# Performance work log

Measured on AMD Instinct MI355X. Metric: run time of the kernel, lower is better.

The kernel has to match this reference:

```python
import jax, jax.numpy as jnp
import numpy as np

N = 20000      # num_nodes / scatter_size
F = 128        # dataset_num_features
H = 8          # heads
HID = 64       # hidden_channels
REP = 512      # represent_features
NCLS = 133     # dataset_num_classes
E = 200000     # num edges (== num synapses)
PTS = 4        # points per synapse
P = E * PTS    # total synapse points

# Eval-mode semantics: dropout = identity; PyG MLP BatchNorm with fresh
# running stats (mean=0, var=1, affine=1/0) = identity. GATConv has no
# edge_dim, so edge_attr does not enter the math (kept as an input for parity).

def _glorot(key, shape):
    fan_in, fan_out = shape[0], shape[-1]
    if len(shape) == 3:  # attention vectors [H, C]: PyG treats as (1, H*C)
        fan_in, fan_out = 1, shape[-2] * shape[-1]
    lim = jnp.sqrt(6.0 / (fan_in + fan_out))
    return jax.random.uniform(key, shape, jnp.float32, -lim, lim)


def setup_inputs() -> dict:
    key = jax.random.key(0)
    ks = jax.random.split(key, 20)
    edge_index = jax.random.randint(ks[0], (2, E), 0, N, dtype=jnp.int32)
    edge_attr = jax.random.normal(ks[1], (E, 1), jnp.float32)
    synapse = jax.random.normal(ks[2], (P, 6), jnp.float32)
    # every synapse (edge) owns PTS points -> no empty segments for max-pool
    synapse_index = (jnp.arange(P, dtype=jnp.int32) // PTS)
    inp = {
        "edge_index": edge_index,
        "edge_attr": edge_attr,
        "synapse": synapse,
        "synapse_index": synapse_index,
        "scatter_size": N,
        # learned node embedding (nn.Parameter, xavier)
        "x_param": _glorot(ks[3], (N, F)),
        # GATConv 1: F -> H*HID
        "W1": _glorot(ks[4], (F, H * HID)),
        "att_src1": _glorot(ks[5], (1, H, HID))[0],
        "att_dst1": _glorot(ks[6], (1, H, HID))[0],
        "b1": jnp.zeros((H * HID,), jnp.float32),
        # GATConv 2: H*HID -> REP, heads=1, concat=False
        "W2": _glorot(ks[7], (H * HID, REP)),
        "att_src2": _glorot(ks[8], (1, 1, REP))[0],
        "att_dst2": _glorot(ks[9], (1, 1, REP))[0],
        "b2": jnp.zeros((REP,), jnp.float32),
        # synapse_encoder MLP([6, 256, 512])
        "We1": _glorot(ks[10], (6, 256)),
        "be1": jnp.zeros((256,), jnp.float32),
        "We2": _glorot(ks[11], (256, 512)),
        "be2": jnp.zeros((512,), jnp.float32),
        # classmodel MLP([1536, 512, 133])
        "Wc1": _glorot(ks[12], (1536, 512)),
        "bc1": jnp.zeros((512,), jnp.float32),
        "Wc2": _glorot(ks[13], (512, NCLS)),
        "bc2": jnp.zeros((NCLS,), jnp.float32),
    }
    return inp


def _gat_conv(x, src, dst, n, W, a_src, a_dst, b, heads, ch, concat):
    # x: [n, Fin]; src/dst already include self-loops (PyG default)
    xl = (x @ W).reshape(n, heads, ch)                 # [n, H, C]
    s = jnp.einsum('nhc,hc->nh', xl, a_src)            # alpha_src
    d = jnp.einsum('nhc,hc->nh', xl, a_dst)            # alpha_dst
    alpha = jax.nn.leaky_relu(s[src] + d[dst], negative_slope=0.2)  # [Ee, H]
    amax = jax.ops.segment_max(alpha, dst, num_segments=n)
    ex = jnp.exp(alpha - amax[dst])
    den = jax.ops.segment_sum(ex, dst, num_segments=n)
    a = ex / (den[dst] + 1e-16)                        # segment softmax
    out = jax.ops.segment_sum(xl[src] * a[:, :, None], dst, num_segments=n)
    out = out.reshape(n, heads * ch) if concat else out.mean(axis=1)
    return out + b


def _scatter_mean(vals, idx, n):
    s = jax.ops.segment_sum(vals, idx, num_segments=n)
    cnt = jax.ops.segment_sum(jnp.ones((vals.shape[0],), vals.dtype), idx, num_segments=n)
    return s / jnp.maximum(cnt, 1.0)[:, None]


def reference(edge_index, edge_attr, synapse, synapse_index, scatter_size,
              x_param, W1, att_src1, att_dst1, b1, W2, att_src2, att_dst2, b2,
              We1, be1, We2, be2, Wc1, bc1, Wc2, bc2):
    n = scatter_size
    loop = jnp.arange(n, dtype=edge_index.dtype)
    src = jnp.concatenate([edge_index[0], loop])   # GATConv adds self-loops
    dst = jnp.concatenate([edge_index[1], loop])

    x = jax.nn.elu(_gat_conv(x_param, src, dst, n, W1, att_src1, att_dst1, b1, H, HID, True))
    x = _gat_conv(x, src, dst, n, W2, att_src2, att_dst2, b2, 1, REP, False)   # [n, REP]

    # global_max_pool over synapse points -> one 6-vec per edge
    x_point = jax.ops.segment_max(synapse, synapse_index, num_segments=E)      # [E, 6]
    x_point = jax.nn.relu(x_point @ We1 + be1) @ We2 + be2                      # [E, 512]

    left = _scatter_mean(x_point, edge_index[0], n)
    right = _scatter_mean(x_point, edge_index[1], n)

    final = jnp.concatenate([x, left, right], axis=1)                           # [n, 1536]
    pred = jax.nn.relu(final @ Wc1 + bc1) @ Wc2 + bc2
    return pred
```

## Files before the change

kernel.cpp:

```cpp
#include <hip/hip_runtime.h>
#include <cstddef>

#define NN   20000
#define FEAT 128
#define NH   8
#define NE   200000
#define EE   220000

typedef _Float16 f16;
typedef _Float16 f16x2 __attribute__((ext_vector_type(2)));
typedef _Float16 f16x4 __attribute__((ext_vector_type(4)));
typedef _Float16 f16x8 __attribute__((ext_vector_type(8)));
typedef float    f32x4 __attribute__((ext_vector_type(4)));

__device__ __forceinline__ float lrelu(float a) { return a > 0.f ? a : 0.2f * a; }
__device__ __forceinline__ float rdlane(float v, int l) {
  return __int_as_float(__builtin_amdgcn_readlane(__float_as_int(v), l));
}

#define QB0 128
#define QB1 (QB0 + 8)
#define QB2 (QB1 + 80)
#define QB3 (QB2 + 64)
#define QB4 (QB3 + 782)
#define QB5 (QB4 + 1250)
__global__ __launch_bounds__(256) void preamble(
    const int* __restrict__ ei, const float* __restrict__ syn,
    const float* __restrict__ W1, const float* __restrict__ xparam,
    const float* __restrict__ W2, const float* __restrict__ We2,
    const float* __restrict__ Wc1, const float* __restrict__ Wc2,
    const float* __restrict__ b2, const float* __restrict__ be2,
    const float* __restrict__ as2, const float* __restrict__ ad2,
    int* __restrict__ dL, int* __restrict__ dR,
    float* __restrict__ xp, f16* __restrict__ W1t, f16* __restrict__ xph,
    f16* __restrict__ WzAt, f16* __restrict__ McatT, f16* __restrict__ Wc2t,
    float* __restrict__ vB, float* __restrict__ vL, float* __restrict__ vR,
    float* __restrict__ ws2, float* __restrict__ wd2)
{
  __shared__ float smem[2112];
  const int b = blockIdx.x, t = threadIdx.x;
  if (b < QB0) {
    float (*As)[68] = (float(*)[68])smem;
    float (*Bs)[64] = (float(*)[64])(smem + 16 * 68);
    const int bb = b;
    const float* A; const float* B; f16* dst; int dstOff, m0, n0;
    if (bb < 64)      { A = W2;  B = Wc1;  dst = WzAt;  dstOff = 0;
                        m0 = (bb >> 3) * 64; n0 = (bb & 7) * 64; }
    else if (bb < 96) { int i = bb - 64; A = We2; B = Wc1 + (size_t)512 * 512;
                        dst = McatT; dstOff = 0;
                        m0 = (i >> 3) * 64; n0 = (i & 7) * 64; }
    else              { int i = bb - 96; A = We2; B = Wc1 + (size_t)1024 * 512;
                        dst = McatT; dstOff = 256;
                        m0 = (i >> 3) * 64; n0 = (i & 7) * 64; }
    const int tx = t & 15, ty = t >> 4;
    float acc[4][4] = {{0.f}};
    float pa[4], pb[4];
#pragma unroll
    for (int i = 0; i < 4; i++) {
      int idx = t + i * 256;
      pa[i] = A[(size_t)(m0 + (idx >> 4)) * 512 + (idx & 15)];
      pb[i] = B[(size_t)(idx >> 6) * 512 + n0 + (idx & 63)];
    }
    for (int k0 = 0; k0 < 512; k0 += 16) {
#pragma unroll
      for (int i = 0; i < 4; i++) {
        int idx = t + i * 256;
        As[idx & 15][idx >> 4] = pa[i];
        Bs[idx >> 6][idx & 63] = pb[i];
      }
      __syncthreads();
      if (k0 + 16 < 512) {
        int kn = k0 + 16;
#pragma unroll
        for (int i = 0; i < 4; i++) {
          int idx = t + i * 256;
          pa[i] = A[(size_t)(m0 + (idx >> 4)) * 512 + kn + (idx & 15)];
          pb[i] = B[(size_t)(kn + (idx >> 6)) * 512 + n0 + (idx & 63)];
        }
      }
#pragma unroll
      for (int kk = 0; kk < 16; kk++) {
        float4 a4 = *(const float4*)&As[kk][ty * 4];
        float4 b4 = *(const float4*)&Bs[kk][tx * 4];
        float av[4] = {a4.x, a4.y, a4.z, a4.w};
        float bv[4] = {b4.x, b4.y, b4.z, b4.w};
#pragma unroll
        for (int i = 0; i < 4; i++)
#pragma unroll
          for (int j = 0; j < 4; j++) acc[i][j] = fmaf(av[i], bv[j], acc[i][j]);
      }
      __syncthreads();
    }
#pragma unroll
    for (int i = 0; i < 4; i++)
#pragma unroll
      for (int j = 0; j < 4; j++)
        dst[(size_t)(n0 + tx * 4 + j) * 512 + dstOff + m0 + ty * 4 + i] = (f16)acc[i][j];
  } else if (b < QB1) {
    int g = (b - QB0) * 256 + t;
    int seg = g >> 9, j = g & 511;
    if (seg == 0) {
      float a = 0.f;
      for (int k = 0; k < 512; k++) a = fmaf(b2[k], Wc1[(size_t)k * 512 + j], a);
      vB[j] = a;
    } else if (seg == 1) {
      float a = 0.f;
      for (int k = 0; k < 512; k++) a = fmaf(be2[k], Wc1[(size_t)(512 + k) * 512 + j], a);
      vL[j] = a;
    } else if (seg == 2) {
      float a = 0.f;
      for (int k = 0; k < 512; k++) a = fmaf(be2[k], Wc1[(size_t)(1024 + k) * 512 + j], a);
      vR[j] = a;
    } else {
      float a = 0.f, c2 = 0.f;
      for (int c = 0; c < 512; c++) {
        float w = W2[(size_t)j * 512 + c];
        a = fmaf(w, as2[c], a);
        c2 = fmaf(w, ad2[c], c2);
      }
      ws2[j] = a; wd2[j] = c2;
    }
  } else if (b < QB2) {
    float (*tile)[33] = (float(*)[33])smem;
    int i0 = b - QB1;
    const int n0 = (i0 % 5) * 32, k0 = (i0 / 5) * 32;
    const int tx = t & 31, ty = t >> 5;
#pragma unroll
    for (int i = 0; i < 4; i++) {
      int k = k0 + ty + i * 8, n = n0 + tx;
      tile[ty + i * 8][tx] = (n < 133) ? Wc2[(size_t)k * 133 + n] : 0.f;
    }
    __syncthreads();
#pragma unroll
    for (int i = 0; i < 4; i++) {
      int n = n0 + ty + i * 8, k = k0 + tx;
      if (n < 133) Wc2t[(size_t)n * 512 + k] = (f16)tile[tx][ty + i * 8];
    }
  } else if (b < QB3) {
    float (*tile)[33] = (float(*)[33])smem;
    int bb = b - QB2;
    const int n0 = (bb & 15) * 32, k0 = (bb >> 4) * 32;
    const int tx = t & 31, ty = t >> 5;
#pragma unroll
    for (int i = 0; i < 4; i++)
      tile[ty + i * 8][tx] = W1[(size_t)(k0 + ty + i * 8) * 512 + n0 + tx];
    __syncthreads();
#pragma unroll
    for (int i = 0; i < 4; i++)
      W1t[(size_t)(n0 + ty + i * 8) * 128 + k0 + tx] = (f16)tile[tx][ty + i * 8];
  } else if (b < QB4) {
    int e = (b - QB3) * 256 + t;
    if (e >= NE) return;
    const float* p = syn + (size_t)e * 24;
    float v[24];
#pragma unroll
    for (int i = 0; i < 6; i++) {
      float4 q = *(const float4*)(p + i * 4);
      v[i*4+0] = q.x; v[i*4+1] = q.y; v[i*4+2] = q.z; v[i*4+3] = q.w;
    }
#pragma unroll
    for (int dd = 0; dd < 6; dd++)
      xp[(size_t)e * 6 + dd] = fmaxf(fmaxf(v[dd], v[6 + dd]), fmaxf(v[12 + dd], v[18 + dd]));
    atomicAdd(&dL[ei[e]], 1);
    atomicAdd(&dR[ei[NE + e]], 1);
  } else {
    int idx = ((b - QB4) * 256 + t) * 8;
    float4 q0 = *(const float4*)(xparam + idx);
    float4 q1 = *(const float4*)(xparam + idx + 4);
    f16x8 o;
    o[0] = (f16)q0.x; o[1] = (f16)q0.y; o[2] = (f16)q0.z; o[3] = (f16)q0.w;
    o[4] = (f16)q1.x; o[5] = (f16)q1.y; o[6] = (f16)q1.z; o[7] = (f16)q1.w;
    *(f16x8*)(xph + idx) = o;
  }
}

__global__ __launch_bounds__(256) void fused1(
    const f16* __restrict__ xph, const f16* __restrict__ W1t, f16* __restrict__ xl1h,
    const float* __restrict__ xp, const float* __restrict__ We1,
    const float* __restrict__ be1,
    const int* __restrict__ oL, const int* __restrict__ eL,
    const int* __restrict__ oR, const int* __restrict__ eR,
    f16* __restrict__ hlrh)
{
  __shared__ __align__(16) f16 smem[7680];
  const int t = threadIdx.x;
  if (blockIdx.x < 1252) {
    f16 (*As)[40] = (f16(*)[40])smem;
    f16 (*Bs)[40] = (f16(*)[40])(smem + 64 * 40);
    const int wave = t >> 6, lane = t & 63;
    const int quad = lane >> 4, mrow = lane & 15;
    const int m0 = (blockIdx.x >> 2) * 64, n0 = (blockIdx.x & 3) * 128;
    f32x4 acc[4][2];
    f32x4 zero4 = {0.f, 0.f, 0.f, 0.f};
#pragma unroll
    for (int i = 0; i < 4; i++)
#pragma unroll
      for (int j = 0; j < 2; j++) acc[i][j] = zero4;
    const int ar = t >> 2, ac = (t & 3) * 8;
    for (int k0 = 0; k0 < FEAT; k0 += 32) {
      {
        int gm = m0 + ar;
        f16x8 v = {0, 0, 0, 0, 0, 0, 0, 0};
        if (gm < NN) v = *(const f16x8*)(xph + (size_t)gm * FEAT + k0 + ac);
        *(f16x8*)&As[ar][ac] = v;
      }
#pragma unroll
      for (int i = 0; i < 2; i++) {
        int idx = t + i * 256;
        int r = idx >> 2, c = (idx & 3) * 8;
        *(f16x8*)&Bs[r][c] = *(const f16x8*)(W1t + (size_t)(n0 + r) * FEAT + k0 + c);
      }
      __syncthreads();
      f16x8 af[4], bf[2];
#pragma unroll
      for (int mt = 0; mt < 4; mt++) af[mt] = *(const f16x8*)&As[mt * 16 + mrow][quad * 8];
#pragma unroll
      for (int nt = 0; nt < 2; nt++) bf[nt] = *(const f16x8*)&Bs[wave * 32 + nt * 16 + mrow][quad * 8];
#pragma unroll
      for (int mt = 0; mt < 4; mt++)
#pragma unroll
        for (int nt = 0; nt < 2; nt++)
          acc[mt][nt] = __builtin_amdgcn_mfma_f32_16x16x32_f16(af[mt], bf[nt], acc[mt][nt], 0, 0, 0);
      __syncthreads();
    }
#pragma unroll
    for (int mt = 0; mt < 4; mt++)
#pragma unroll
      for (int nt = 0; nt < 2; nt++) {
        int col = n0 + wave * 32 + nt * 16 + mrow;
#pragma unroll
        for (int reg = 0; reg < 4; reg++) {
          int row = m0 + mt * 16 + quad * 4 + reg;
          if (row < NN) xl1h[(size_t)row * 512 + col] = (f16)acc[mt][nt][reg];
        }
      }
  } else {
    const int wave = t >> 6, lane = t & 63;
    const int w = (blockIdx.x - 1252) * 4 + wave;
    float4 wv[6];
#pragma unroll
    for (int j = 0; j < 6; j++) wv[j] = *(const float4*)(We1 + j * 256 + 4 * lane);
    const float4 bv = *(const float4*)(be1 + 4 * lane);
#pragma unroll 1
    for (int i = 0; i < 4; i++) {
      const int b = w + i * 10000;
      const int* off; const int* lst; int n;
      if (b < NN) { off = oL; lst = eL; n = b; } else { off = oR; lst = eR; n = b - NN; }
      const int beg = off[n], deg = off[n + 1] - beg;
      float a0 = 0.f, a1 = 0.f, a2 = 0.f, a3 = 0.f;
      for (int base = 0; base < deg; base += 32) {
        const int m = min(32, deg - base);
        float x0 = 0.f, x1 = 0.f, x2 = 0.f, x3 = 0.f, x4 = 0.f, x5 = 0.f;
        if (lane < m) {
          const int e = lst[beg + base + lane];
          const float* pr = xp + (size_t)e * 6;
          float2 p0 = *(const float2*)pr;
          float2 p1 = *(const float2*)(pr + 2);
          float2 p2 = *(const float2*)(pr + 4);
          x0 = p0.x; x1 = p0.y; x2 = p1.x; x3 = p1.y; x4 = p2.x; x5 = p2.y;
        }
        const int ms = __builtin_amdgcn_readfirstlane(m);
        for (int s = 0; s < ms; s++) {
          const float f0 = rdlane(x0, s), f1 = rdlane(x1, s), f2 = rdlane(x2, s);
          const float f3 = rdlane(x3, s), f4 = rdlane(x4, s), f5 = rdlane(x5, s);
          float v0 = bv.x, v1 = bv.y, v2 = bv.z, v3 = bv.w;
          v0 = fmaf(f0, wv[0].x, v0); v1 = fmaf(f0, wv[0].y, v1);
          v2 = fmaf(f0, wv[0].z, v2); v3 = fmaf(f0, wv[0].w, v3);
          v0 = fmaf(f1, wv[1].x, v0); v1 = fmaf(f1, wv[1].y, v1);
          v2 = fmaf(f1, wv[1].z, v2); v3 = fmaf(f1, wv[1].w, v3);
          v0 = fmaf(f2, wv[2].x, v0); v1 = fmaf(f2, wv[2].y, v1);
          v2 = fmaf(f2, wv[2].z, v2); v3 = fmaf(f2, wv[2].w, v3);
          v0 = fmaf(f3, wv[3].x, v0); v1 = fmaf(f3, wv[3].y, v1);
          v2 = fmaf(f3, wv[3].z, v2); v3 = fmaf(f3, wv[3].w, v3);
          v0 = fmaf(f4, wv[4].x, v0); v1 = fmaf(f4, wv[4].y, v1);
          v2 = fmaf(f4, wv[4].z, v2); v3 = fmaf(f4, wv[4].w, v3);
          v0 = fmaf(f5, wv[5].x, v0); v1 = fmaf(f5, wv[5].y, v1);
          v2 = fmaf(f5, wv[5].z, v2); v3 = fmaf(f5, wv[5].w, v3);
          a0 += fmaxf(v0, 0.f); a1 += fmaxf(v1, 0.f);
          a2 += fmaxf(v2, 0.f); a3 += fmaxf(v3, 0.f);
        }
      }
      const float rn = deg > 0 ? 1.f / (float)deg : 0.f;
      f16x4 o;
      o[0] = (f16)(a0 * rn); o[1] = (f16)(a1 * rn);
      o[2] = (f16)(a2 * rn); o[3] = (f16)(a3 * rn);
      *(f16x4*)(hlrh + (size_t)b * 256 + 4 * lane) = o;
    }
  }
}

__global__ __launch_bounds__(256) void fused2(
    const f16* __restrict__ x1h, const f16* __restrict__ WzAt, f16* __restrict__ zh,
    const f16* __restrict__ hlrh, const f16* __restrict__ McatT,
    const int* __restrict__ degL, const int* __restrict__ degR,
    const float* __restrict__ bc1, const float* __restrict__ vB,
    const float* __restrict__ vL, const float* __restrict__ vR, f16* __restrict__ Ph)
{
  __shared__ __align__(16) f16 smem[7680];
  const int t = threadIdx.x;
  f16 (*As)[40] = (f16(*)[40])smem;
  f16 (*Bs)[40] = (f16(*)[40])(smem + 64 * 40);
  const bool isZ = blockIdx.x < 1252;
  const int bb = isZ ? blockIdx.x : blockIdx.x - 1252;
  const int wave = t >> 6, lane = t & 63;
  const int quad = lane >> 4, mrow = lane & 15;
  const int m0 = (bb >> 2) * 64, n0 = (bb & 3) * 128;
  f32x4 acc[4][2];
  f32x4 zero4 = {0.f, 0.f, 0.f, 0.f};
#pragma unroll
  for (int i = 0; i < 4; i++)
#pragma unroll
    for (int j = 0; j < 2; j++) acc[i][j] = zero4;
  const int ar = t >> 2, ac = (t & 3) * 8;
  const f16* Bt = isZ ? WzAt : McatT;
  for (int k0 = 0; k0 < 512; k0 += 32) {
    {
      int gm = m0 + ar;
      f16x8 v = {0, 0, 0, 0, 0, 0, 0, 0};
      if (gm < NN) {
        if (isZ) v = *(const f16x8*)(x1h + (size_t)gm * 512 + k0 + ac);
        else {
          size_t row = (k0 >> 8) ? (size_t)(NN + gm) : (size_t)gm;
          v = *(const f16x8*)(hlrh + row * 256 + (k0 & 255) + ac);
        }
      }
      *(f16x8*)&As[ar][ac] = v;
    }
#pragma unroll
    for (int i = 0; i < 2; i++) {
      int idx = t + i * 256;
      int r = idx >> 2, c = (idx & 3) * 8;
      *(f16x8*)&Bs[r][c] = *(const f16x8*)(Bt + (size_t)(n0 + r) * 512 + k0 + c);
    }
    __syncthreads();
    f16x8 af[4], bf[2];
#pragma unroll
    for (int mt = 0; mt < 4; mt++) af[mt] = *(const f16x8*)&As[mt * 16 + mrow][quad * 8];
#pragma unroll
    for (int nt = 0; nt < 2; nt++) bf[nt] = *(const f16x8*)&Bs[wave * 32 + nt * 16 + mrow][quad * 8];
#pragma unroll
    for (int mt = 0; mt < 4; mt++)
#pragma unroll
      for (int nt = 0; nt < 2; nt++)
        acc[mt][nt] = __builtin_amdgcn_mfma_f32_16x16x32_f16(af[mt], bf[nt], acc[mt][nt], 0, 0, 0);
    __syncthreads();
  }
  if (isZ) {
#pragma unroll
    for (int mt = 0; mt < 4; mt++)
#pragma unroll
      for (int nt = 0; nt < 2; nt++) {
        int col = n0 + wave * 32 + nt * 16 + mrow;
#pragma unroll
        for (int reg = 0; reg < 4; reg++) {
          int row = m0 + mt * 16 + quad * 4 + reg;
          if (row < NN) zh[(size_t)row * 512 + col] = (f16)acc[mt][nt][reg];
        }
      }
  } else {
#pragma unroll
    for (int mt = 0; mt < 4; mt++)
#pragma unroll
      for (int nt = 0; nt < 2; nt++) {
        int col = n0 + wave * 32 + nt * 16 + mrow;
        float bb2 = bc1[col] + vB[col];
        float vl = vL[col], vr = vR[col];
#pragma unroll
        for (int reg = 0; reg < 4; reg++) {
          int row = m0 + mt * 16 + quad * 4 + reg;
          if (row >= NN) continue;
          float v = acc[mt][nt][reg] + bb2;
          if (degL[row] > 0) v += vl;
          if (degR[row] > 0) v += vr;
          Ph[(size_t)row * 512 + col] = (f16)v;
        }
      }
  }
}

__global__ __launch_bounds__(256) void mfma_out(
    const f16* __restrict__ A, const f16* __restrict__ Bt,
    const float* __restrict__ bias, float* __restrict__ C, int M)
{
  __shared__ __align__(16) f16 As[64][40];
  __shared__ __align__(16) f16 Bs[128][40];
  const int t = threadIdx.x;
  const int wave = t >> 6, lane = t & 63;
  const int quad = lane >> 4, mrow = lane & 15;
  const int m0 = blockIdx.y * 64, n0 = blockIdx.x * 128;
  f32x4 acc[4][2];
  f32x4 zero4 = {0.f, 0.f, 0.f, 0.f};
#pragma unroll
  for (int i = 0; i < 4; i++)
#pragma unroll
    for (int j = 0; j < 2; j++) acc[i][j] = zero4;
  const int ar = t >> 2, ac = (t & 3) * 8;
  for (int k0 = 0; k0 < 512; k0 += 32) {
    {
      int gm = m0 + ar;
      f16x8 v = {0, 0, 0, 0, 0, 0, 0, 0};
      if (gm < M) v = *(const f16x8*)(A + (size_t)gm * 512 + k0 + ac);
      *(f16x8*)&As[ar][ac] = v;
    }
#pragma unroll
    for (int i = 0; i < 2; i++) {
      int idx = t + i * 256;
      int r = idx >> 2, c = (idx & 3) * 8;
      f16x8 v = {0, 0, 0, 0, 0, 0, 0, 0};
      if (n0 + r < 133) v = *(const f16x8*)(Bt + (size_t)(n0 + r) * 512 + k0 + c);
      *(f16x8*)&Bs[r][c] = v;
    }
    __syncthreads();
    f16x8 af[4], bf[2];
#pragma unroll
    for (int mt = 0; mt < 4; mt++) af[mt] = *(const f16x8*)&As[mt * 16 + mrow][quad * 8];
#pragma unroll
    for (int nt = 0; nt < 2; nt++) bf[nt] = *(const f16x8*)&Bs[wave * 32 + nt * 16 + mrow][quad * 8];
#pragma unroll
    for (int mt = 0; mt < 4; mt++)
#pragma unroll
      for (int nt = 0; nt < 2; nt++)
        acc[mt][nt] = __builtin_amdgcn_mfma_f32_16x16x32_f16(af[mt], bf[nt], acc[mt][nt], 0, 0, 0);
    __syncthreads();
  }
#pragma unroll
  for (int mt = 0; mt < 4; mt++)
#pragma unroll
    for (int nt = 0; nt < 2; nt++) {
      int col = n0 + wave * 32 + nt * 16 + mrow;
      if (col >= 133) continue;
      float bb = bias[col];
#pragma unroll
      for (int reg = 0; reg < 4; reg++) {
        int row = m0 + mt * 16 + quad * 4 + reg;
        if (row < M) C[(size_t)row * 133 + col] = acc[mt][nt][reg] + bb;
      }
    }
}

__global__ __launch_bounds__(1024) void scan_csr(
    const int* __restrict__ dL, const int* __restrict__ dR,
    int* __restrict__ oL, int* __restrict__ oR, int* __restrict__ oA)
{
  const int b = blockIdx.x;
  const int* deg = b == 0 ? dL : dR;
  __shared__ int part[1024];
  const int t = threadIdx.x;
  const int chunk = 20;
  int base = t * chunk;
  int sum = 0;
  for (int i = 0; i < chunk; i++) { int idx = base + i; if (idx < NN) sum += deg[idx]; }
  part[t] = sum;
  __syncthreads();
  for (int o = 1; o < 1024; o <<= 1) {
    int v = (t >= o) ? part[t - o] : 0;
    __syncthreads();
    part[t] += v;
    __syncthreads();
  }
  int run = part[t] - sum;
  if (b == 0) {
    for (int i = 0; i < chunk; i++) {
      int idx = base + i;
      if (idx < NN) { oL[idx] = run; run += deg[idx]; }
    }
    if (t == 0) oL[NN] = part[1023];
  } else {
    for (int i = 0; i < chunk; i++) {
      int idx = base + i;
      if (idx < NN) { oR[idx] = run; oA[idx] = run + idx; run += deg[idx]; }
    }
    if (t == 0) { oR[NN] = part[1023]; oA[NN] = part[1023] + NN; }
  }
}

__global__ __launch_bounds__(256) void fill_csr(
    const int* __restrict__ ei,
    const int* __restrict__ oL, const int* __restrict__ oR, const int* __restrict__ oA,
    int* __restrict__ cL, int* __restrict__ cR,
    int* __restrict__ eL, int* __restrict__ eR, int* __restrict__ snA)
{
  int e = blockIdx.x * 256 + threadIdx.x;
  if (e >= EE) return;
  if (e < NE) {
    int s = ei[e], d = ei[NE + e];
    int p = atomicAdd(&cL[s], 1); eL[oL[s] + p] = e;
    p = atomicAdd(&cR[d], 1);
    eR[oR[d] + p] = e;
    snA[oA[d] + 1 + p] = s;
  } else {
    int n = e - NE;
    snA[oA[n]] = n;
  }
}

__global__ __launch_bounds__(256) void attn_dots1(
    const f16* __restrict__ xlh, const float* __restrict__ asrc,
    const float* __restrict__ adst, float* __restrict__ s, float* __restrict__ d)
{
  int gid = blockIdx.x * 256 + threadIdx.x;
  if (gid >= NN * NH) return;
  int n = gid >> 3, h = gid & 7;
  const f16x2* row = (const f16x2*)(xlh + (size_t)n * 512 + h * 64);
  const float* a1 = asrc + h * 64;
  const float* a2 = adst + h * 64;
  float ss = 0.f, dd = 0.f;
#pragma unroll 8
  for (int j = 0; j < 32; j++) {
    f16x2 p = row[j];
    float v0 = (float)p[0], v1 = (float)p[1];
    ss += v0 * a1[2 * j] + v1 * a1[2 * j + 1];
    dd += v0 * a2[2 * j] + v1 * a2[2 * j + 1];
  }
  s[gid] = ss; d[gid] = dd;
}

__global__ __launch_bounds__(256) void gat_gather1(
    const int* __restrict__ snA, const int* __restrict__ offA,
    const float* __restrict__ s1, const float* __restrict__ d1,
    const f16* __restrict__ xlh, const float* __restrict__ b1,
    const float* __restrict__ ws2, const float* __restrict__ wd2,
    f16* __restrict__ x1h, float* __restrict__ s2, float* __restrict__ d2)
{
  __shared__ int sns[32];
  __shared__ float wls[256];
  __shared__ float red[256], redD[256];
  const int n = blockIdx.x, t = threadIdx.x;
  const int hw = t & 7;
  const int slot = t >> 3;
  const int hf = t >> 5;
  const int beg = offA[n], end = offA[n + 1];
  const int deg = end - beg;
  const float dnw = d1[n * 8 + hw];
  float a0 = 0.f, a1v = 0.f, denp = 0.f;
  for (int base = 0; base < deg; base += 32) {
    int m = min(32, deg - base);
    if (t < 32) sns[t] = (t < m) ? snA[beg + base + t] : 0;
    __syncthreads();
    {
      float w = 0.f;
      if (slot < m) w = __expf(lrelu(s1[sns[slot] * 8 + hw] + dnw));
      wls[t] = w;
      denp += w;
    }
    __syncthreads();
    int m8 = (m + 7) & ~7;
    for (int k = 0; k < m8; k += 8) {
      int ss[8]; float ww[8]; f16x2 pp[8];
#pragma unroll
      for (int u = 0; u < 8; u++) { ss[u] = sns[k + u]; ww[u] = wls[(k + u) * 8 + hf]; }
#pragma unroll
      for (int u = 0; u < 8; u++) pp[u] = *(const f16x2*)(xlh + (size_t)ss[u] * 512 + 2 * t);
#pragma unroll
      for (int u = 0; u < 8; u++) {
        a0  = fmaf(ww[u], (float)pp[u][0], a0);
        a1v = fmaf(ww[u], (float)pp[u][1], a1v);
      }
    }
    __syncthreads();
  }
  red[t] = denp;
  __syncthreads();
  for (int off = 128; off >= 8; off >>= 1) {
    if (t < off) red[t] += red[t + off];
    __syncthreads();
  }
  float rh = 1.f / (red[hf] + 1e-16f);
  __syncthreads();
  float v0 = a0 * rh + b1[2 * t], v1 = a1v * rh + b1[2 * t + 1];
  v0 = v0 > 0.f ? v0 : (__expf(v0) - 1.f);
  v1 = v1 > 0.f ? v1 : (__expf(v1) - 1.f);
  f16x2 o; o[0] = (f16)v0; o[1] = (f16)v1;
  *(f16x2*)(x1h + (size_t)n * 512 + 2 * t) = o;
  red[t]  = v0 * ws2[2 * t] + v1 * ws2[2 * t + 1];
  redD[t] = v0 * wd2[2 * t] + v1 * wd2[2 * t + 1];
  __syncthreads();
  for (int off = 128; off > 0; off >>= 1) {
    if (t < off) { red[t] += red[t + off]; redD[t] += redD[t + off]; }
    __syncthreads();
  }
  if (t == 0) { s2[n] = red[0]; d2[n] = redD[0]; }
}

__global__ __launch_bounds__(256) void gat_gather2(
    const int* __restrict__ snA, const int* __restrict__ offA,
    const float* __restrict__ s2, const float* __restrict__ d2,
    const f16* __restrict__ zh, const f16* __restrict__ Ph,
    f16* __restrict__ h2h)
{
  __shared__ int sns[32];
  __shared__ float wls[32];
  __shared__ float den_sh;
  const int n = blockIdx.x, t = threadIdx.x;
  const int beg = offA[n], end = offA[n + 1];
  const int deg = end - beg;
  const float dn = d2[n];
  float a0 = 0.f, a1v = 0.f, denp = 0.f;
  for (int base = 0; base < deg; base += 32) {
    int m = min(32, deg - base);
    if (t < 32) {
      int sn = (t < m) ? snA[beg + base + t] : 0;
      float w = (t < m) ? __expf(lrelu(s2[sn] + dn)) : 0.f;
      sns[t] = sn;
      wls[t] = w;
      denp += w;
    }
    __syncthreads();
    int m8 = (m + 7) & ~7;
    for (int k = 0; k < m8; k += 8) {
      int ss[8]; float ww[8]; f16x2 pp[8];
#pragma unroll
      for (int u = 0; u < 8; u++) { ss[u] = sns[k + u]; ww[u] = wls[k + u]; }
#pragma unroll
      for (int u = 0; u < 8; u++) pp[u] = *(const f16x2*)(zh + (size_t)ss[u] * 512 + 2 * t);
#pragma unroll
      for (int u = 0; u < 8; u++) {
        a0  = fmaf(ww[u], (float)pp[u][0], a0);
        a1v = fmaf(ww[u], (float)pp[u][1], a1v);
      }
    }
    __syncthreads();
  }
  if (t < 64) {
    denp += __shfl_xor(denp, 16);
    denp += __shfl_xor(denp, 8);
    denp += __shfl_xor(denp, 4);
    denp += __shfl_xor(denp, 2);
    denp += __shfl_xor(denp, 1);
    if (t == 0) den_sh = denp;
  }
  __syncthreads();
  float rn = 1.f / (den_sh + 1e-16f);
  f16x2 pv = *(const f16x2*)(Ph + (size_t)n * 512 + 2 * t);
  float v0 = fmaxf(a0  * rn + (float)pv[0], 0.f);
  float v1 = fmaxf(a1v * rn + (float)pv[1], 0.f);
  f16x2 o; o[0] = (f16)v0; o[1] = (f16)v1;
  *(f16x2*)(h2h + (size_t)n * 512 + 2 * t) = o;
}

extern "C" void kernel_launch(void* const* d_in, const int* in_sizes, int n_in,
                              void* d_out, int out_size, void* d_ws, size_t ws_size,
                              hipStream_t stream) {
  const int*   edge_index = (const int*)d_in[0];
  const float* synapse    = (const float*)d_in[2];
  const float* x_param = (const float*)d_in[5];
  const float* W1      = (const float*)d_in[6];
  const float* as1     = (const float*)d_in[7];
  const float* ad1     = (const float*)d_in[8];
  const float* b1      = (const float*)d_in[9];
  const float* W2      = (const float*)d_in[10];
  const float* as2     = (const float*)d_in[11];
  const float* ad2     = (const float*)d_in[12];
  const float* b2      = (const float*)d_in[13];
  const float* We1     = (const float*)d_in[14];
  const float* be1     = (const float*)d_in[15];
  const float* We2     = (const float*)d_in[16];
  const float* be2     = (const float*)d_in[17];
  const float* Wc1     = (const float*)d_in[18];
  const float* bc1     = (const float*)d_in[19];
  const float* Wc2     = (const float*)d_in[20];
  const float* bc2     = (const float*)d_in[21];
  float* out_p = (float*)d_out;

  char* p = (char*)d_ws;
  float* xp    = (float*)p; p += (size_t)NE * 6 * 4;
  float* s1    = (float*)p; p += (size_t)NN * 8 * 4;
  float* d1    = (float*)p; p += (size_t)NN * 8 * 4;
  float* s2    = (float*)p; p += (size_t)NN * 4;
  float* d2    = (float*)p; p += (size_t)NN * 4;
  float* vB    = (float*)p; p += 512 * 4;
  float* vL    = (float*)p; p += 512 * 4;
  float* vR    = (float*)p; p += 512 * 4;
  float* ws2   = (float*)p; p += 512 * 4;
  float* wd2   = (float*)p; p += 512 * 4;
  f16* xph     = (f16*)p; p += (size_t)NN * FEAT * 2;
  f16* xl1h    = (f16*)p; p += (size_t)NN * 512 * 2;
  f16* x1h     = (f16*)p; p += (size_t)NN * 512 * 2;
  f16* zh      = (f16*)p; p += (size_t)NN * 512 * 2;
  f16* h2h     = (f16*)p; p += (size_t)NN * 512 * 2;
  f16* Phb     = (f16*)p; p += (size_t)NN * 512 * 2;
  f16* hlrh    = (f16*)p; p += (size_t)2 * NN * 256 * 2;
  f16* W1t     = (f16*)p; p += (size_t)512 * FEAT * 2;
  f16* WzAt    = (f16*)p; p += (size_t)512 * 512 * 2;
  f16* McatT   = (f16*)p; p += (size_t)512 * 512 * 2;
  f16* Wc2t    = (f16*)p; p += (size_t)133 * 512 * 2;
  int* degL    = (int*)p;
  int* degR    = degL + NN;
  int* curL    = degR + NN;
  int* curR    = curL + NN;
  int* offL    = curR + NN;
  int* offR    = offL + NN + 1;
  int* offA    = offR + NN + 1;
  int* edgeL   = offA + NN + 1;
  int* edgeR   = edgeL + NE;
  int* snA     = edgeR + NE;

  hipMemsetAsync(degL, 0, (size_t)4 * NN * sizeof(int), stream);

  preamble<<<QB5, 256, 0, stream>>>(
      edge_index, synapse, W1, x_param, W2, We2, Wc1, Wc2, b2, be2, as2, ad2,
      degL, degR, xp, W1t, xph, WzAt, McatT, Wc2t, vB, vL, vR, ws2, wd2);
  scan_csr<<<2, 1024, 0, stream>>>(degL, degR, offL, offR, offA);
  fill_csr<<<(EE + 255) / 256, 256, 0, stream>>>(edge_index, offL, offR, offA,
                                                 curL, curR, edgeL, edgeR, snA);
  fused1<<<1252 + 2500, 256, 0, stream>>>(xph, W1t, xl1h, xp, We1, be1,
                                          offL, edgeL, offR, edgeR, hlrh);
  attn_dots1<<<(NN * NH + 255) / 256, 256, 0, stream>>>(xl1h, as1, ad1, s1, d1);
  gat_gather1<<<NN, 256, 0, stream>>>(snA, offA, s1, d1, xl1h, b1, ws2, wd2,
                                      x1h, s2, d2);
  fused2<<<2504, 256, 0, stream>>>(x1h, WzAt, zh, hlrh, McatT,
                                   degL, degR, bc1, vB, vL, vR, Phb);
  gat_gather2<<<NN, 256, 0, stream>>>(snA, offA, s2, d2, zh, Phb, h2h);
  mfma_out<<<dim3(2, 313), 256, 0, stream>>>(h2h, Wc2t, bc2, out_p, NN);
}
```

Before: 439.5 us.

## Double-buffer LDS tiles with register prefetch and XCD-aware block remap in fused2

The fused2 GEMM loop now prefetches the next K-slice of A and B into registers while MFMAs run on the current slice. It ping-pongs between two LDS buffers, so the trailing __syncthreads per iteration can be dropped. Block indices are also remapped by (blockIdx & 7)*313 + (blockIdx>>3), so consecutive logical tiles land on the same XCD for better L2 reuse. The cost is doubled LDS per block and extra live registers, which may lower occupancy.

```diff
diff --git a/kernel.cpp b/kernel.cpp
--- a/kernel.cpp
+++ b/kernel.cpp
@@ -296,12 +296,11 @@
     const float* __restrict__ bc1, const float* __restrict__ vB,
     const float* __restrict__ vL, const float* __restrict__ vR, f16* __restrict__ Ph)
 {
-  __shared__ __align__(16) f16 smem[7680];
+  __shared__ __align__(16) f16 smem[15360];
   const int t = threadIdx.x;
-  f16 (*As)[40] = (f16(*)[40])smem;
-  f16 (*Bs)[40] = (f16(*)[40])(smem + 64 * 40);
-  const bool isZ = blockIdx.x < 1252;
-  const int bb = isZ ? blockIdx.x : blockIdx.x - 1252;
+  const int logical = (blockIdx.x & 7) * 313 + (blockIdx.x >> 3);
+  const bool isZ = logical < 1252;
+  const int bb = isZ ? logical : logical - 1252;
   const int wave = t >> 6, lane = t & 63;
   const int quad = lane >> 4, mrow = lane & 15;
   const int m0 = (bb >> 2) * 64, n0 = (bb & 3) * 128;
@@ -312,27 +311,38 @@
 #pragma unroll
     for (int j = 0; j < 2; j++) acc[i][j] = zero4;
   const int ar = t >> 2, ac = (t & 3) * 8;
+  const int gm = m0 + ar;
   const f16* Bt = isZ ? WzAt : McatT;
-  for (int k0 = 0; k0 < 512; k0 += 32) {
-    {
-      int gm = m0 + ar;
-      f16x8 v = {0, 0, 0, 0, 0, 0, 0, 0};
-      if (gm < NN) {
-        if (isZ) v = *(const f16x8*)(x1h + (size_t)gm * 512 + k0 + ac);
-        else {
-          size_t row = (k0 >> 8) ? (size_t)(NN + gm) : (size_t)gm;
-          v = *(const f16x8*)(hlrh + row * 256 + (k0 & 255) + ac);
-        }
-      }
-      *(f16x8*)&As[ar][ac] = v;
-    }
-#pragma unroll
-    for (int i = 0; i < 2; i++) {
-      int idx = t + i * 256;
-      int r = idx >> 2, c = (idx & 3) * 8;
-      *(f16x8*)&Bs[r][c] = *(const f16x8*)(Bt + (size_t)(n0 + r) * 512 + k0 + c);
-    }
-    __syncthreads();
+
+  auto loadA = [&](int k0) -> f16x8 {
+    f16x8 v = {0, 0, 0, 0, 0, 0, 0, 0};
+    if (gm < NN) {
+      if (isZ) v = *(const f16x8*)(x1h + (size_t)gm * 512 + k0 + ac);
+      else {
+        size_t row = (k0 >> 8) ? (size_t)(NN + gm) : (size_t)gm;
+        v = *(const f16x8*)(hlrh + row * 256 + (k0 & 255) + ac);
+      }
+    }
+    return v;
+  };
+  auto loadB = [&](int k0, int i) -> f16x8 {
+    int idx = t + i * 256;
+    return *(const f16x8*)(Bt + (size_t)(n0 + (idx >> 2)) * 512 + k0 + ((idx & 3) * 8));
+  };
+
+  f16x8 ra = loadA(0), rb0 = loadB(0, 0), rb1 = loadB(0, 1);
+#pragma unroll 1
+  for (int it = 0; it < 16; ++it) {
+    f16 (*As)[40] = (f16(*)[40])(smem + (it & 1) * 7680);
+    f16 (*Bs)[40] = (f16(*)[40])(smem + (it & 1) * 7680 + 2560);
+    *(f16x8*)&As[ar][ac] = ra;
+    *(f16x8*)&Bs[t >> 2][(t & 3) * 8] = rb0;
+    *(f16x8*)&Bs[(t + 256) >> 2][(t & 3) * 8] = rb1;
+    __syncthreads();
+    if (it < 15) {
+      int kn = (it + 1) * 32;
+      ra = loadA(kn); rb0 = loadB(kn, 0); rb1 = loadB(kn, 1);
+    }
     f16x8 af[4], bf[2];
 #pragma unroll
     for (int mt = 0; mt < 4; mt++) af[mt] = *(const f16x8*)&As[mt * 16 + mrow][quad * 8];
@@ -343,7 +353,6 @@
 #pragma unroll
       for (int nt = 0; nt < 2; nt++)
         acc[mt][nt] = __builtin_amdgcn_mfma_f32_16x16x32_f16(af[mt], bf[nt], acc[mt][nt], 0, 0, 0);
-    __syncthreads();
   }
   if (isZ) {
 #pragma unroll
```

Measured after the change: 431.5 us. About the same (-1.8%).
